# Performance work log

Hardware: AMD Instinct MI355X
Metric: run time of the kernel (lower is better)

The kernel has to match this reference:

```python
import jax, jax.numpy as jnp
import numpy as np

B, S, C = 4, 2048, 1024
E, H = 1024, 16
D = E // H  # head_dim = 64


def setup_inputs() -> dict:
    key = jax.random.key(0)
    k1, k2, k3, k4, k5 = jax.random.split(key, 5)
    s = 1.0 / np.sqrt(C)
    return {
        "x": jax.random.normal(k1, (B, S, C), dtype=jnp.float32),
        "w_qkv": jax.random.uniform(k2, (C, 3 * E), minval=-s, maxval=s, dtype=jnp.float32),
        "b_qkv": jax.random.uniform(k3, (3 * E,), minval=-s, maxval=s, dtype=jnp.float32),
        "w_out": jax.random.uniform(k4, (E, E), minval=-1.0 / np.sqrt(E), maxval=1.0 / np.sqrt(E), dtype=jnp.float32),
        "b_out": jax.random.uniform(k5, (E,), minval=-1.0 / np.sqrt(E), maxval=1.0 / np.sqrt(E), dtype=jnp.float32),
    }


def reference(x, w_qkv, b_qkv, w_out, b_out):
    b, s, _ = x.shape
    qkv = x @ w_qkv + b_qkv                      # [B,S,3E]
    qkv = qkv.reshape(b, s, 3, H, D)
    q = qkv[:, :, 0].transpose(0, 2, 1, 3)       # [B,H,S,D]
    k = qkv[:, :, 1].transpose(0, 2, 1, 3)
    v = qkv[:, :, 2].transpose(0, 2, 1, 3)
    scale = jnp.asarray(D, x.dtype) ** 0.5
    scores = jnp.einsum("bhqd,bhkd->bhqk", q, k) / scale
    attn = jax.nn.softmax(scores, axis=-1)       # dropout is identity in eval mode
    out = jnp.einsum("bhqk,bhkd->bhqd", attn, v)
    out = out.transpose(0, 2, 1, 3).reshape(b, s, E)
    return out @ w_out + b_out
```

## Files before the change

### kernel.cpp

```cpp
#include <hip/hip_runtime.h>


typedef _Float16 f16;
typedef f16 f16x2 __attribute__((ext_vector_type(2)));
typedef f16 f16x4 __attribute__((ext_vector_type(4)));
typedef f16 f16x8 __attribute__((ext_vector_type(8)));
typedef float f32x4 __attribute__((ext_vector_type(4)));

typedef const __attribute__((address_space(1))) void* gas_ptr;
typedef __attribute__((address_space(3))) void* lds_ptr;

__device__ __forceinline__ void load_lds16(const void* g, void* s) {
  __builtin_amdgcn_global_load_lds((gas_ptr)g, (lds_ptr)s, 16, 0, 0);
}

__device__ __forceinline__ f32x4 mfma16(f16x8 a, f16x8 b, f32x4 c) {
  return __builtin_amdgcn_mfma_f32_16x16x32_f16(a, b, c, 0, 0, 0);
}

__device__ __forceinline__ f16x2 pk2(float a, float b) {
  return __builtin_bit_cast(f16x2, __builtin_amdgcn_cvt_pkrtz(a, b));
}

__global__ __launch_bounds__(256) void cvt_x(const float* __restrict__ in, f16* __restrict__ out) {
  int i = blockIdx.x * 256 + threadIdx.x;
  const float4* p = (const float4*)in;
  float4 a = p[2 * i], b = p[2 * i + 1];
  f16x8 o;
  o[0] = (f16)a.x; o[1] = (f16)a.y; o[2] = (f16)a.z; o[3] = (f16)a.w;
  o[4] = (f16)b.x; o[5] = (f16)b.y; o[6] = (f16)b.z; o[7] = (f16)b.w;
  *(f16x8*)(out + 8 * (long)i) = o;
}

__global__ __launch_bounds__(256) void tconv(const float* __restrict__ in, f16* __restrict__ out,
                                             int R, int C) {
  __shared__ float t[32][33];
  int c0 = blockIdx.x * 32, r0 = blockIdx.y * 32;
  int tx = threadIdx.x, ty = threadIdx.y;
#pragma unroll
  for (int j = 0; j < 4; ++j)
    t[ty + 8 * j][tx] = in[(long)(r0 + ty + 8 * j) * C + c0 + tx];
  __syncthreads();
#pragma unroll
  for (int j = 0; j < 4; ++j)
    out[(long)(c0 + ty + 8 * j) * R + r0 + tx] = (f16)t[tx][ty + 8 * j];
}

__global__ __launch_bounds__(256) void qkv_gemm(const f16* __restrict__ A, const f16* __restrict__ BT,
                                                const float* __restrict__ bias,
                                                f16* __restrict__ Qs, f16* __restrict__ Kk,
                                                f16* __restrict__ Vt) {
  __shared__ __align__(16) f16 lA[128 * 32];
  __shared__ __align__(16) f16 lB[128 * 32];
  const int K = 1024;
  int tid = threadIdx.x, w = tid >> 6, lane = tid & 63, l16 = lane & 15, quad = lane >> 4;
  int wm = (w >> 1) * 64, wn = (w & 1) * 64;
  int id = blockIdx.y * gridDim.x + blockIdx.x;
  int cpx = (gridDim.x * gridDim.y) >> 3;
  int swz = (id & 7) * cpx + (id >> 3);
  int bx = swz & 63, by = swz >> 6;
  int blockM = bx * 128, blockN = by * 128;
  f32x4 acc[4][4] = {};

  for (int k0 = 0; k0 < K; k0 += 32) {
    __syncthreads();
#pragma unroll
    for (int i = 0; i < 2; ++i) {
      int c = (i * 4 + w) * 64 + lane;
      load_lds16(A + (blockM + (c >> 2)) * K + k0 + (c & 3) * 8, lA + (i * 4 + w) * 512);
      load_lds16(BT + (blockN + (c >> 2)) * K + k0 + (c & 3) * 8, lB + (i * 4 + w) * 512);
    }
    __syncthreads();
    f16x8 af[4], bf[4];
#pragma unroll
    for (int mb = 0; mb < 4; ++mb) af[mb] = *(const f16x8*)&lA[(wm + mb * 16 + l16) * 32 + quad * 8];
#pragma unroll
    for (int nb = 0; nb < 4; ++nb) bf[nb] = *(const f16x8*)&lB[(wn + nb * 16 + l16) * 32 + quad * 8];
#pragma unroll
    for (int mb = 0; mb < 4; ++mb)
#pragma unroll
      for (int nb = 0; nb < 4; ++nb)
        acc[mb][nb] = mfma16(af[mb], bf[nb], acc[mb][nb]);
  }

  int which = by >> 3;
  const float SCALE = 0.18033688011112042f;
#pragma unroll
  for (int nb = 0; nb < 4; ++nb) {
    int col = blockN + wn + nb * 16 + l16;
    int hd = col & 1023, h = hd >> 6, d = hd & 63;
    float bv = bias[col];
#pragma unroll
    for (int mb = 0; mb < 4; ++mb) {
      int row0 = blockM + wm + mb * 16 + quad * 4;
      int b = row0 >> 11, s0 = row0 & 2047;
      if (which == 2) {
        f16x2 a = pk2(acc[mb][nb][0] + bv, acc[mb][nb][1] + bv);
        f16x2 c = pk2(acc[mb][nb][2] + bv, acc[mb][nb][3] + bv);
        *(f16x4*)&Vt[((b * 16 + h) * 64 + d) * 2048 + s0] =
            __builtin_shufflevector(a, c, 0, 1, 2, 3);
      } else if (which == 0) {
#pragma unroll
        for (int r = 0; r < 4; ++r)
          Qs[((b * 16 + h) * 2048 + s0 + r) * 64 + d] = (f16)((acc[mb][nb][r] + bv) * SCALE);
      } else {
#pragma unroll
        for (int r = 0; r < 4; ++r)
          Kk[((b * 16 + h) * 2048 + s0 + r) * 64 + d] = (f16)(acc[mb][nb][r] + bv);
      }
    }
  }
}

__global__ __launch_bounds__(512, 4) void attn(const f16* __restrict__ Qs, const f16* __restrict__ Kk,
                                               const f16* __restrict__ Vt, f16* __restrict__ ctx) {
  __shared__ __align__(16) f16 lK[2][64 * 72];
  __shared__ __align__(16) f16 lV[2][64 * 72];
  int id = blockIdx.y * gridDim.x + blockIdx.x;
  int swz = (id & 7) * 64 + (id >> 3);
  int qt = swz & 7, bh = swz >> 3;
  int tid = threadIdx.x, lane = tid & 63, l16 = lane & 15, quad = lane >> 4;
  int w = tid >> 6;
  const f16* Qbase = Qs + ((long)bh * 2048 + qt * 256 + w * 32) * 64;
  const f16* Kbh = Kk + (long)bh * 2048 * 64;
  const f16* Vbh = Vt + (long)bh * 64 * 2048;

  f16x8 qf[2][2];
#pragma unroll
  for (int rb = 0; rb < 2; ++rb)
#pragma unroll
    for (int ks = 0; ks < 2; ++ks)
      qf[rb][ks] = *(const f16x8*)(Qbase + (rb * 16 + l16) * 64 + ks * 32 + quad * 8);

  f32x4 of[2][4] = {};
  f32x4 osum[2] = {};
  const f16 one = (f16)1.f;
  const f16x8 vone8 = {one, one, one, one, one, one, one, one};

  int rs = tid >> 3, o = (tid & 7) * 8;
  int koff = o & 31;
  int cperm = (o & 32) + ((koff & 12) << 1) + ((koff >> 4) << 2);

  {
    *(float4*)&lK[0][rs * 72 + o] = *(const float4*)(Kbh + rs * 64 + o);
    float4 pv = *(const float4*)(Vbh + (long)rs * 2048 + o);
    f16x8 v8 = __builtin_bit_cast(f16x8, pv);
    *(f16x4*)&lV[0][rs * 72 + cperm] = __builtin_shufflevector(v8, v8, 0, 1, 2, 3);
    *(f16x4*)&lV[0][rs * 72 + cperm + 8] = __builtin_shufflevector(v8, v8, 4, 5, 6, 7);
  }
  __syncthreads();

  for (int kt = 0; kt < 32; ++kt) {
    int cur = kt & 1, nxt = cur ^ 1;

    float4 pk0, pv0;
    if (kt < 31) {
      int kb0 = (kt + 1) * 64;
      pk0 = *(const float4*)(Kbh + (kb0 + rs) * 64 + o);
      pv0 = *(const float4*)(Vbh + (long)rs * 2048 + kb0 + o);
    }

    __builtin_amdgcn_s_setprio(1);
#pragma unroll
    for (int kp = 0; kp < 2; ++kp) {
      f16x4 pah[2][2];
#pragma unroll
      for (int kbh = 0; kbh < 2; ++kbh) {
        int kb = kp * 2 + kbh;
        f16x8 kf0 = *(const f16x8*)&lK[cur][(kb * 16 + l16) * 72 + quad * 8];
        f16x8 kf1 = *(const f16x8*)&lK[cur][(kb * 16 + l16) * 72 + 32 + quad * 8];
#pragma unroll
        for (int rb = 0; rb < 2; ++rb) {
          f32x4 z = {};
          z = mfma16(kf0, qf[rb][0], z);
          z = mfma16(kf1, qf[rb][1], z);
          float p0 = __builtin_amdgcn_exp2f(z[0]);
          float p1 = __builtin_amdgcn_exp2f(z[1]);
          float p2 = __builtin_amdgcn_exp2f(z[2]);
          float p3 = __builtin_amdgcn_exp2f(z[3]);
          pah[rb][kbh] = __builtin_shufflevector(pk2(p0, p1), pk2(p2, p3), 0, 1, 2, 3);
        }
      }
      f16x8 pa[2];
      pa[0] = __builtin_shufflevector(pah[0][0], pah[0][1], 0, 1, 2, 3, 4, 5, 6, 7);
      pa[1] = __builtin_shufflevector(pah[1][0], pah[1][1], 0, 1, 2, 3, 4, 5, 6, 7);

#pragma unroll
      for (int db = 0; db < 4; ++db) {
        f16x8 vf = *(const f16x8*)&lV[cur][(db * 16 + l16) * 72 + kp * 32 + quad * 8];
#pragma unroll
        for (int rb = 0; rb < 2; ++rb)
          of[rb][db] = mfma16(pa[rb], vf, of[rb][db]);
      }
#pragma unroll
      for (int rb = 0; rb < 2; ++rb)
        osum[rb] = mfma16(pa[rb], vone8, osum[rb]);
    }
    __builtin_amdgcn_s_setprio(0);

    if (kt < 31) {
      *(float4*)&lK[nxt][rs * 72 + o] = pk0;
      f16x8 v8 = __builtin_bit_cast(f16x8, pv0);
      *(f16x4*)&lV[nxt][rs * 72 + cperm] = __builtin_shufflevector(v8, v8, 0, 1, 2, 3);
      *(f16x4*)&lV[nxt][rs * 72 + cperm + 8] = __builtin_shufflevector(v8, v8, 4, 5, 6, 7);
      __syncthreads();
    }
  }

  int b = bh >> 4, h = bh & 15;
  long token0 = (long)b * 2048 + qt * 256 + w * 32;
#pragma unroll
  for (int rb = 0; rb < 2; ++rb) {
    float inv[4];
#pragma unroll
    for (int r = 0; r < 4; ++r) inv[r] = 1.0f / osum[rb][r];
#pragma unroll
    for (int db = 0; db < 4; ++db)
#pragma unroll
      for (int r = 0; r < 4; ++r)
        ctx[(token0 + rb * 16 + quad * 4 + r) * 1024 + h * 64 + db * 16 + l16] =
            (f16)(of[rb][db][r] * inv[r]);
  }
}

__global__ __launch_bounds__(256) void proj_gemm(const f16* __restrict__ A, const f16* __restrict__ BT,
                                                 const float* __restrict__ bias,
                                                 float* __restrict__ out) {
  __shared__ __align__(16) f16 lA[128 * 32];
  __shared__ __align__(16) f16 lB[128 * 32];
  const int K = 1024;
  int tid = threadIdx.x, w = tid >> 6, lane = tid & 63, l16 = lane & 15, quad = lane >> 4;
  int wm = (w >> 1) * 64, wn = (w & 1) * 64;
  int id = blockIdx.y * gridDim.x + blockIdx.x;
  int cpx = (gridDim.x * gridDim.y) >> 3;
  int swz = (id & 7) * cpx + (id >> 3);
  int bx = swz & 63, by = swz >> 6;
  int blockM = bx * 128, blockN = by * 128;
  f32x4 acc[4][4] = {};

  for (int k0 = 0; k0 < K; k0 += 32) {
    __syncthreads();
#pragma unroll
    for (int i = 0; i < 2; ++i) {
      int c = (i * 4 + w) * 64 + lane;
      load_lds16(A + (blockM + (c >> 2)) * K + k0 + (c & 3) * 8, lA + (i * 4 + w) * 512);
      load_lds16(BT + (blockN + (c >> 2)) * K + k0 + (c & 3) * 8, lB + (i * 4 + w) * 512);
    }
    __syncthreads();
    f16x8 af[4], bf[4];
#pragma unroll
    for (int mb = 0; mb < 4; ++mb) af[mb] = *(const f16x8*)&lA[(wm + mb * 16 + l16) * 32 + quad * 8];
#pragma unroll
    for (int nb = 0; nb < 4; ++nb) bf[nb] = *(const f16x8*)&lB[(wn + nb * 16 + l16) * 32 + quad * 8];
#pragma unroll
    for (int mb = 0; mb < 4; ++mb)
#pragma unroll
      for (int nb = 0; nb < 4; ++nb)
        acc[mb][nb] = mfma16(af[mb], bf[nb], acc[mb][nb]);
  }

#pragma unroll
  for (int nb = 0; nb < 4; ++nb) {
    int col = blockN + wn + nb * 16 + l16;
    float bv = bias[col];
#pragma unroll
    for (int mb = 0; mb < 4; ++mb) {
#pragma unroll
      for (int r = 0; r < 4; ++r) {
        int row = blockM + wm + mb * 16 + quad * 4 + r;
        out[(long)row * 1024 + col] = acc[mb][nb][r] + bv;
      }
    }
  }
}

extern "C" void kernel_launch(void* const* d_in, const int* in_sizes, int n_in,
                              void* d_out, int out_size, void* d_ws, size_t ws_size,
                              hipStream_t stream) {
  const float* x     = (const float*)d_in[0];
  const float* w_qkv = (const float*)d_in[1];
  const float* b_qkv = (const float*)d_in[2];
  const float* w_out = (const float*)d_in[3];
  const float* b_out = (const float*)d_in[4];
  float* out = (float*)d_out;

  char* ws = (char*)d_ws;
  f16* xh    = (f16*)(ws);
  f16* ctx   = (f16*)(ws);
  f16* wqkvT = (f16*)(ws + 16777216);
  f16* woutT = (f16*)(ws + 23068672);
  f16* Qs    = (f16*)(ws + 25165824);
  f16* Kk    = (f16*)(ws + 41943040);
  f16* Vt    = (f16*)(ws + 58720256);

  cvt_x<<<4096, 256, 0, stream>>>(x, xh);
  tconv<<<dim3(96, 32), dim3(32, 8), 0, stream>>>(w_qkv, wqkvT, 1024, 3072);
  tconv<<<dim3(32, 32), dim3(32, 8), 0, stream>>>(w_out, woutT, 1024, 1024);
  qkv_gemm<<<dim3(64, 24), 256, 0, stream>>>(xh, wqkvT, b_qkv, Qs, Kk, Vt);
  attn<<<dim3(8, 64), 512, 0, stream>>>(Qs, Kk, Vt, ctx);
  proj_gemm<<<dim3(64, 8), 256, 0, stream>>>(ctx, woutT, b_out, out);
}
```

Measured before the change: 274.1 us.

## Double GEMM K-tile to 64 with XOR-swizzled LDS and XCD-grouped block mapping

```diff
diff --git a/kernel.cpp b/kernel.cpp
--- a/kernel.cpp
+++ b/kernel.cpp
@@ -50,37 +50,44 @@
                                                 const float* __restrict__ bias,
                                                 f16* __restrict__ Qs, f16* __restrict__ Kk,
                                                 f16* __restrict__ Vt) {
-  __shared__ __align__(16) f16 lA[128 * 32];
-  __shared__ __align__(16) f16 lB[128 * 32];
+  __shared__ __align__(16) f16 lA[128 * 64];
+  __shared__ __align__(16) f16 lB[128 * 64];
   const int K = 1024;
   int tid = threadIdx.x, w = tid >> 6, lane = tid & 63, l16 = lane & 15, quad = lane >> 4;
   int wm = (w >> 1) * 64, wn = (w & 1) * 64;
   int id = blockIdx.y * gridDim.x + blockIdx.x;
-  int cpx = (gridDim.x * gridDim.y) >> 3;
-  int swz = (id & 7) * cpx + (id >> 3);
-  int bx = swz & 63, by = swz >> 6;
+  int xcd = id & 7, cch = id >> 3;
+  int bx = xcd * 8 + (cch & 7), by = cch >> 3;
   int blockM = bx * 128, blockN = by * 128;
+  int sw = l16 & 7;
   f32x4 acc[4][4] = {};
 
-  for (int k0 = 0; k0 < K; k0 += 32) {
+  for (int k0 = 0; k0 < K; k0 += 64) {
     __syncthreads();
 #pragma unroll
-    for (int i = 0; i < 2; ++i) {
-      int c = (i * 4 + w) * 64 + lane;
-      load_lds16(A + (blockM + (c >> 2)) * K + k0 + (c & 3) * 8, lA + (i * 4 + w) * 512);
-      load_lds16(BT + (blockN + (c >> 2)) * K + k0 + (c & 3) * 8, lB + (i * 4 + w) * 512);
+    for (int i = 0; i < 4; ++i) {
+      int c = i * 256 + tid;
+      int row = c >> 3;
+      int sc = (c & 7) ^ (row & 7);
+      load_lds16(A + (blockM + row) * K + k0 + sc * 8, lA + c * 8);
+      load_lds16(BT + (blockN + row) * K + k0 + sc * 8, lB + c * 8);
     }
     __syncthreads();
-    f16x8 af[4], bf[4];
-#pragma unroll
-    for (int mb = 0; mb < 4; ++mb) af[mb] = *(const f16x8*)&lA[(wm + mb * 16 + l16) * 32 + quad * 8];
-#pragma unroll
-    for (int nb = 0; nb < 4; ++nb) bf[nb] = *(const f16x8*)&lB[(wn + nb * 16 + l16) * 32 + quad * 8];
-#pragma unroll
-    for (int mb = 0; mb < 4; ++mb)
+#pragma unroll
+    for (int ks = 0; ks < 2; ++ks) {
+      f16x8 af[4], bf[4];
+#pragma unroll
+      for (int mb = 0; mb < 4; ++mb)
+        af[mb] = *(const f16x8*)&lA[(wm + mb * 16 + l16) * 64 + ((ks * 4 + quad) ^ sw) * 8];
 #pragma unroll
       for (int nb = 0; nb < 4; ++nb)
-        acc[mb][nb] = mfma16(af[mb], bf[nb], acc[mb][nb]);
+        bf[nb] = *(const f16x8*)&lB[(wn + nb * 16 + l16) * 64 + ((ks * 4 + quad) ^ sw) * 8];
+#pragma unroll
+      for (int mb = 0; mb < 4; ++mb)
+#pragma unroll
+        for (int nb = 0; nb < 4; ++nb)
+          acc[mb][nb] = mfma16(af[mb], bf[nb], acc[mb][nb]);
+    }
   }
 
   int which = by >> 3;
@@ -226,37 +233,44 @@
 __global__ __launch_bounds__(256) void proj_gemm(const f16* __restrict__ A, const f16* __restrict__ BT,
                                                  const float* __restrict__ bias,
                                                  float* __restrict__ out) {
-  __shared__ __align__(16) f16 lA[128 * 32];
-  __shared__ __align__(16) f16 lB[128 * 32];
+  __shared__ __align__(16) f16 lA[128 * 64];
+  __shared__ __align__(16) f16 lB[128 * 64];
   const int K = 1024;
   int tid = threadIdx.x, w = tid >> 6, lane = tid & 63, l16 = lane & 15, quad = lane >> 4;
   int wm = (w >> 1) * 64, wn = (w & 1) * 64;
   int id = blockIdx.y * gridDim.x + blockIdx.x;
-  int cpx = (gridDim.x * gridDim.y) >> 3;
-  int swz = (id & 7) * cpx + (id >> 3);
-  int bx = swz & 63, by = swz >> 6;
+  int xcd = id & 7, cch = id >> 3;
+  int bx = xcd * 8 + (cch & 7), by = cch >> 3;
   int blockM = bx * 128, blockN = by * 128;
+  int sw = l16 & 7;
   f32x4 acc[4][4] = {};
 
-  for (int k0 = 0; k0 < K; k0 += 32) {
+  for (int k0 = 0; k0 < K; k0 += 64) {
     __syncthreads();
 #pragma unroll
-    for (int i = 0; i < 2; ++i) {
-      int c = (i * 4 + w) * 64 + lane;
-      load_lds16(A + (blockM + (c >> 2)) * K + k0 + (c & 3) * 8, lA + (i * 4 + w) * 512);
-      load_lds16(BT + (blockN + (c >> 2)) * K + k0 + (c & 3) * 8, lB + (i * 4 + w) * 512);
+    for (int i = 0; i < 4; ++i) {
+      int c = i * 256 + tid;
+      int row = c >> 3;
+      int sc = (c & 7) ^ (row & 7);
+      load_lds16(A + (blockM + row) * K + k0 + sc * 8, lA + c * 8);
+      load_lds16(BT + (blockN + row) * K + k0 + sc * 8, lB + c * 8);
     }
     __syncthreads();
-    f16x8 af[4], bf[4];
-#pragma unroll
-    for (int mb = 0; mb < 4; ++mb) af[mb] = *(const f16x8*)&lA[(wm + mb * 16 + l16) * 32 + quad * 8];
-#pragma unroll
-    for (int nb = 0; nb < 4; ++nb) bf[nb] = *(const f16x8*)&lB[(wn + nb * 16 + l16) * 32 + quad * 8];
-#pragma unroll
-    for (int mb = 0; mb < 4; ++mb)
+#pragma unroll
+    for (int ks = 0; ks < 2; ++ks) {
+      f16x8 af[4], bf[4];
+#pragma unroll
+      for (int mb = 0; mb < 4; ++mb)
+        af[mb] = *(const f16x8*)&lA[(wm + mb * 16 + l16) * 64 + ((ks * 4 + quad) ^ sw) * 8];
 #pragma unroll
       for (int nb = 0; nb < 4; ++nb)
-        acc[mb][nb] = mfma16(af[mb], bf[nb], acc[mb][nb]);
+        bf[nb] = *(const f16x8*)&lB[(wn + nb * 16 + l16) * 64 + ((ks * 4 + quad) ^ sw) * 8];
+#pragma unroll
+      for (int mb = 0; mb < 4; ++mb)
+#pragma unroll
+        for (int nb = 0; nb < 4; ++nb)
+          acc[mb][nb] = mfma16(af[mb], bf[nb], acc[mb][nb]);
+    }
   }
 
 #pragma unroll
```

After: 267.1 us. -2.5%, faster.
